# Optimization experiments

Hardware: AMD Instinct MI355X
Metric: run time of the kernel (lower is better)

## Reference

```python
import jax, jax.numpy as jnp
import numpy as np

N_NODES = 50000
N_EDGES = 800000
N_GRAPHS = 512
NNF = 32      # num_node_features
EAD = 16      # edge_attr_dim
UD = 32       # u_dim
H = 64        # hidden_dim
OUT = 1


def _w(key, shape, scale=0.05):
    return (jax.random.normal(key, shape, dtype=jnp.float32) * scale)


def setup_inputs() -> dict:
    key = jax.random.key(0)
    ks = iter(jax.random.split(key, 64))
    inp = {
        "x": jax.random.normal(next(ks), (N_NODES, NNF), dtype=jnp.float32),
        "edge_attr": jax.random.normal(next(ks), (N_EDGES, EAD), dtype=jnp.float32),
        "u": jax.random.normal(next(ks), (N_GRAPHS, UD), dtype=jnp.float32),
        # edge MLPs: Linear(EAD,H), ReLU, Linear(H,H)
        "em1_w1": _w(next(ks), (EAD, H)), "em1_b1": jnp.zeros((H,), jnp.float32),
        "em1_w2": _w(next(ks), (H, H)),   "em1_b2": jnp.zeros((H,), jnp.float32),
        "em2_w1": _w(next(ks), (EAD, H)), "em2_b1": jnp.zeros((H,), jnp.float32),
        "em2_w2": _w(next(ks), (H, H)),   "em2_b2": jnp.zeros((H,), jnp.float32),
        # layer-1 GINEConvs (a,b,c stacked on leading axis 3):
        # internal edge projection lin: Linear(H -> NNF); nn: Linear(NNF,H),ReLU,Linear(H,H)
        "c1_lin_w": _w(next(ks), (3, H, NNF)), "c1_lin_b": jnp.zeros((3, NNF), jnp.float32),
        "c1_w1": _w(next(ks), (3, NNF, H)),    "c1_b1": jnp.zeros((3, H), jnp.float32),
        "c1_w2": _w(next(ks), (3, H, H)),      "c1_b2": jnp.zeros((3, H), jnp.float32),
        # layer-2 GINEConvs: lin: Linear(H->H); nn: Linear(H,H),ReLU,Linear(H,H)
        "c2_lin_w": _w(next(ks), (3, H, H)), "c2_lin_b": jnp.zeros((3, H), jnp.float32),
        "c2_w1": _w(next(ks), (3, H, H)),    "c2_b1": jnp.zeros((3, H), jnp.float32),
        "c2_w2": _w(next(ks), (3, H, H)),    "c2_b2": jnp.zeros((3, H), jnp.float32),
        # fusion linears and head
        "lin1_w": _w(next(ks), (3 * H, H)), "lin1_b": jnp.zeros((H,), jnp.float32),
        "lin2_w": _w(next(ks), (3 * H, H)), "lin2_b": jnp.zeros((H,), jnp.float32),
        "fc_w": _w(next(ks), (H + UD, OUT)), "fc_b": jnp.zeros((OUT,), jnp.float32),
        "edge_index": jax.random.randint(next(ks), (2, N_EDGES), 0, N_NODES, dtype=jnp.int64),
        "batch": jnp.sort(jax.random.randint(next(ks), (N_NODES,), 0, N_GRAPHS, dtype=jnp.int64)),
    }
    return inp


def _gine(x, src, dst, ea, lin_w, lin_b, w1, b1, w2, b2):
    # GINEConv (eps=0): out = nn(x + sum_j relu(x_j + lin(e_ij)))
    m = jax.nn.relu(x[src] + ea @ lin_w + lin_b)          # [E, d_x]
    agg = jax.ops.segment_sum(m, dst, num_segments=x.shape[0])
    h = x + agg
    return jax.nn.relu(h @ w1 + b1) @ w2 + b2             # [N, H]


def _triple(x, src, dst, ea, lw, lb, w1, b1, w2, b2):
    # run 3 parallel GINEConvs (a,b,c) and concat features
    outs = jax.vmap(_gine, in_axes=(None, None, None, None, 0, 0, 0, 0, 0, 0))(
        x, src, dst, ea, lw, lb, w1, b1, w2, b2)          # [3, N, H]
    return outs.transpose(1, 0, 2).reshape(x.shape[0], -1)  # [N, 3H]


def reference(x, edge_attr, u,
              em1_w1, em1_b1, em1_w2, em1_b2,
              em2_w1, em2_b1, em2_w2, em2_b2,
              c1_lin_w, c1_lin_b, c1_w1, c1_b1, c1_w2, c1_b2,
              c2_lin_w, c2_lin_b, c2_w1, c2_b1, c2_w2, c2_b2,
              lin1_w, lin1_b, lin2_w, lin2_b, fc_w, fc_b,
              edge_index, batch):
    src, dst = edge_index[0], edge_index[1]
    # layer 1
    ea1 = jax.nn.relu(edge_attr @ em1_w1 + em1_b1) @ em1_w2 + em1_b2
    h = _triple(x, src, dst, ea1, c1_lin_w, c1_lin_b, c1_w1, c1_b1, c1_w2, c1_b2)
    h = jax.nn.relu(h @ lin1_w + lin1_b)                  # [N, H]
    # layer 2
    ea2 = jax.nn.relu(edge_attr @ em2_w1 + em2_b1) @ em2_w2 + em2_b2
    h = _triple(h, src, dst, ea2, c2_lin_w, c2_lin_b, c2_w1, c2_b1, c2_w2, c2_b2)
    h = jax.nn.relu(h @ lin2_w + lin2_b)                  # [N, H]
    # global mean pool per graph
    sums = jax.ops.segment_sum(h, batch, num_segments=N_GRAPHS)
    cnt = jax.ops.segment_sum(jnp.ones((h.shape[0], 1), h.dtype), batch, num_segments=N_GRAPHS)
    pooled = sums / jnp.maximum(cnt, 1.0)                 # [G, H]
    return jnp.concatenate([pooled, u], axis=-1) @ fc_w + fc_b  # [G, 1]
```

## Files before the change

### kernel.cpp

```cpp
#include <hip/hip_runtime.h>
#include <hip/hip_bf16.h>

#define N_NODES  50000
#define N_EDGES  800000
#define N_GRAPHS 512
#define ECHUNK   400000
#define NTILES   3125

typedef short bf16x8 __attribute__((ext_vector_type(8)));
typedef float f32x4  __attribute__((ext_vector_type(4)));
typedef float f32x2  __attribute__((ext_vector_type(2)));

constexpr size_t B_CNT  = 0;
constexpr size_t ZERO_BYTES = 200192;
constexpr size_t B_OFF  = 200192;
constexpr size_t B_CUR  = 400384;
constexpr size_t B_BSUM = 600576;
constexpr size_t B_SSRC = 601600;
constexpr size_t B_SEID = 3801600;
constexpr size_t B_FR2  = 7001600;
constexpr size_t B_AGG2 = 7134720;
constexpr size_t B_Q    = 45534720;
constexpr size_t B_H1   = 199134720;
constexpr size_t B_H2   = 211934720;
constexpr size_t B_FOLD = 224734720;
constexpr size_t B_FRAG = 224908416;
constexpr int F_V1H = 0;
constexpr int F_B1F = 6144;
constexpr int F_V2H = 6240;
constexpr int F_B2F = 18528;
constexpr int F_U1  = 18720;
constexpr int F_UB1 = 31008;
constexpr int F_U2  = 31072;
constexpr int F_UB2 = 43360;
constexpr int FOLD_TOTAL = 43424;
constexpr int FR_W1E1 = 0;
constexpr int FR_W1E2 = 2048;
constexpr int FR_V1   = 4096;
constexpr int FR_V2   = 10240;
constexpr int FOLD2_TOTAL = 22528;
constexpr int FR3_M1W = 0;
constexpr int FR3_M1U = 6144;
constexpr int FR3_M2W = 18432;
constexpr int FR3_M2U = 30720;
constexpr int FOLD3_TOTAL = 43008;

__device__ inline unsigned short bf16u(float x) {
    unsigned int ua = __float_as_uint(x);
    return (unsigned short)((ua + 0x7FFFu + ((ua >> 16) & 1u)) >> 16);
}
__device__ inline unsigned int packbf2(float a, float b) {
    unsigned int ua = __float_as_uint(a), ub = __float_as_uint(b);
    return ((ua + 0x7FFFu + ((ua >> 16) & 1u)) >> 16) |
           ((ub + 0x7FFFu + ((ub >> 16) & 1u)) & 0xFFFF0000u);
}
__device__ inline unsigned short pkfp8(float a, float b) {
    return (unsigned short)__builtin_amdgcn_cvt_pk_fp8_f32(a, b, 0, false);
}
__device__ inline f32x2 unpkfp8(unsigned short us) {
    return __builtin_amdgcn_cvt_pk_f32_fp8((int)us, false);
}

__global__ __launch_bounds__(256) void fold_kernel(
    const float* __restrict__ em1_w2, const float* __restrict__ em1_b2,
    const float* __restrict__ em2_w2, const float* __restrict__ em2_b2,
    const float* __restrict__ c1_lin_w, const float* __restrict__ c1_lin_b,
    const float* __restrict__ c2_lin_w, const float* __restrict__ c2_lin_b,
    const float* __restrict__ c1_w2, const float* __restrict__ c1_b2,
    const float* __restrict__ c2_w2, const float* __restrict__ c2_b2,
    const float* __restrict__ lin1_w, const float* __restrict__ lin1_b,
    const float* __restrict__ lin2_w, const float* __restrict__ lin2_b,
    float* __restrict__ fw)
{
    int idx = blockIdx.x * 256 + threadIdx.x;
    if (idx >= FOLD_TOTAL) return;
    int r = idx;
    if (r < 6144) {
        int k = r / 96, c = r % 96, i = c / 32, j = c % 32;
        float s = 0.f;
        for (int m = 0; m < 64; m++) s = fmaf(em1_w2[k * 64 + m], c1_lin_w[i * 2048 + m * 32 + j], s);
        fw[F_V1H + r] = s; return;
    }
    r -= 6144;
    if (r < 96) {
        int i = r / 32, j = r % 32;
        float s = c1_lin_b[r];
        for (int m = 0; m < 64; m++) s = fmaf(em1_b2[m], c1_lin_w[i * 2048 + m * 32 + j], s);
        fw[F_B1F + r] = s; return;
    }
    r -= 96;
    if (r < 12288) {
        int k = r / 192, c = r % 192, i = c / 64, j = c % 64;
        float s = 0.f;
        for (int m = 0; m < 64; m++) s = fmaf(em2_w2[k * 64 + m], c2_lin_w[i * 4096 + m * 64 + j], s);
        fw[F_V2H + r] = s; return;
    }
    r -= 12288;
    if (r < 192) {
        int i = r / 64, j = r % 64;
        float s = c2_lin_b[r];
        for (int m = 0; m < 64; m++) s = fmaf(em2_b2[m], c2_lin_w[i * 4096 + m * 64 + j], s);
        fw[F_B2F + r] = s; return;
    }
    r -= 192;
    if (r < 12288) {
        int i = r / 4096, k = (r / 64) % 64, j = r % 64;
        float s = 0.f;
        for (int m = 0; m < 64; m++) s = fmaf(c1_w2[i * 4096 + k * 64 + m], lin1_w[(i * 64 + m) * 64 + j], s);
        fw[F_U1 + r] = s; return;
    }
    r -= 12288;
    if (r < 64) {
        float s = lin1_b[r];
        for (int i = 0; i < 3; i++)
            for (int m = 0; m < 64; m++) s = fmaf(c1_b2[i * 64 + m], lin1_w[(i * 64 + m) * 64 + r], s);
        fw[F_UB1 + r] = s; return;
    }
    r -= 64;
    if (r < 12288) {
        int i = r / 4096, k = (r / 64) % 64, j = r % 64;
        float s = 0.f;
        for (int m = 0; m < 64; m++) s = fmaf(c2_w2[i * 4096 + k * 64 + m], lin2_w[(i * 64 + m) * 64 + j], s);
        fw[F_U2 + r] = s; return;
    }
    r -= 12288;
    {
        float s = lin2_b[r];
        for (int i = 0; i < 3; i++)
            for (int m = 0; m < 64; m++) s = fmaf(c2_b2[i * 64 + m], lin2_w[(i * 64 + m) * 64 + r], s);
        fw[F_UB2 + r] = s; return;
    }
}

__global__ __launch_bounds__(256) void fold2_kernel(
    const float* __restrict__ em1_w1, const float* __restrict__ em2_w1,
    const float* __restrict__ fw, unsigned short* __restrict__ fr)
{
    int idx = blockIdx.x * 256 + threadIdx.x;
    if (idx >= FOLD2_TOTAL) return;
    if (idx < 4096) {
        const float* w = (idx < 2048) ? em1_w1 : em2_w1;
        int r = idx & 2047;
        int tt = r >> 9, lane = (r >> 3) & 63, j = r & 7;
        int q = lane >> 4, k = q * 8 + j, m = tt * 16 + (lane & 15);
        fr[idx] = (k < 16) ? bf16u(w[k * 64 + m]) : (unsigned short)0;
        return;
    }
    if (idx < 10240) {
        int r = idx - 4096;
        int nt = r / 1024, ka = (r >> 9) & 1, lane = (r >> 3) & 63, j = r & 7;
        int q = lane >> 4;
        int t = 32 * ka + 16 * (j >> 2) + 4 * q + (j & 3);
        int n = nt * 16 + (lane & 15);
        fr[idx] = bf16u(fw[F_V1H + t * 96 + n]);
        return;
    }
    {
        int r = idx - 10240;
        int nt = r / 1024, ka = (r >> 9) & 1, lane = (r >> 3) & 63, j = r & 7;
        int q = lane >> 4;
        int t = 32 * ka + 16 * (j >> 2) + 4 * q + (j & 3);
        int n = nt * 16 + (lane & 15);
        fr[idx] = bf16u(fw[F_V2H + t * 192 + n]);
        return;
    }
}

__global__ __launch_bounds__(256) void fold3_kernel(
    const float* __restrict__ c1_w1, const float* __restrict__ c2_w1,
    const float* __restrict__ fw, unsigned short* __restrict__ fr2)
{
    int idx = blockIdx.x * 256 + threadIdx.x;
    if (idx >= FOLD3_TOTAL) return;
    if (idx < 6144) {
        int i = idx / 2048, r = idx % 2048;
        int tt = r >> 9, lane = (r >> 3) & 63, jj = r & 7;
        int k = (lane >> 4) * 8 + jj, m = tt * 16 + (lane & 15);
        fr2[FR3_M1W + idx] = bf16u(c1_w1[i * 2048 + k * 64 + m]);
        return;
    }
    if (idx < 18432) {
        int r = idx - 6144;
        int i = r / 4096, r2 = r % 4096;
        int b = r2 >> 10, ka = (r2 >> 9) & 1, lane = (r2 >> 3) & 63, jj = r2 & 7;
        int t = 32 * ka + 16 * (jj >> 2) + 4 * (lane >> 4) + (jj & 3);
        int n = b * 16 + (lane & 15);
        fr2[FR3_M1U + r] = bf16u(fw[F_U1 + i * 4096 + t * 64 + n]);
        return;
    }
    if (idx < 30720) {
        int r = idx - 18432;
        int i = r / 4096, r2 = r % 4096;
        int tt = r2 >> 10, ka = (r2 >> 9) & 1, lane = (r2 >> 3) & 63, jj = r2 & 7;
        int k = ka * 32 + (lane >> 4) * 8 + jj, m = tt * 16 + (lane & 15);
        fr2[FR3_M2W + r] = bf16u(c2_w1[i * 4096 + k * 64 + m]);
        return;
    }
    {
        int r = idx - 30720;
        int i = r / 4096, r2 = r % 4096;
        int b = r2 >> 10, ka = (r2 >> 9) & 1, lane = (r2 >> 3) & 63, jj = r2 & 7;
        int t = 32 * ka + 16 * (jj >> 2) + 4 * (lane >> 4) + (jj & 3);
        int n = b * 16 + (lane & 15);
        fr2[FR3_M2U + r] = bf16u(fw[F_U2 + i * 4096 + t * 64 + n]);
        return;
    }
}

__global__ __launch_bounds__(256) void hist_kernel(const int* __restrict__ ei, int* __restrict__ cnt) {
    int e = blockIdx.x * 256 + threadIdx.x;
    if (e < N_EDGES) atomicAdd(&cnt[ei[N_EDGES + e]], 1);
}

__global__ __launch_bounds__(256) void scan1_kernel(const int* __restrict__ cnt,
                                                    int* __restrict__ off, int* __restrict__ bsum) {
    __shared__ int sh[256];
    int t = threadIdx.x, i = blockIdx.x * 256 + t;
    int v = (i < N_NODES) ? cnt[i] : 0;
    sh[t] = v; __syncthreads();
    for (int d = 1; d < 256; d <<= 1) {
        int add = (t >= d) ? sh[t - d] : 0;
        __syncthreads();
        sh[t] += add;
        __syncthreads();
    }
    if (i < N_NODES) off[i] = sh[t] - v;
    if (t == 255) bsum[blockIdx.x] = sh[255];
}

__global__ __launch_bounds__(256) void scan2_kernel(int* __restrict__ bsum) {
    __shared__ int sh[256];
    int t = threadIdx.x;
    int v = (t < 196) ? bsum[t] : 0;
    sh[t] = v; __syncthreads();
    for (int d = 1; d < 256; d <<= 1) {
        int add = (t >= d) ? sh[t - d] : 0;
        __syncthreads();
        sh[t] += add;
        __syncthreads();
    }
    bsum[t] = sh[t] - v;
}

__global__ __launch_bounds__(256) void scan3_kernel(int* __restrict__ off, const int* __restrict__ bsum,
                                                    int* __restrict__ cur) {
    int i = blockIdx.x * 256 + threadIdx.x;
    if (i < N_NODES) {
        int o = off[i] + bsum[i >> 8];
        off[i] = o;
        cur[i] = o;
    }
    if (i == 0) off[N_NODES] = N_EDGES;
}

__global__ __launch_bounds__(256) void scatter_kernel(const int* __restrict__ ei, int* __restrict__ cur,
                                                      int* __restrict__ ssrc, int* __restrict__ seid) {
    int e = blockIdx.x * 256 + threadIdx.x;
    if (e >= N_EDGES) return;
    int d = ei[N_EDGES + e];
    int p = atomicAdd(&cur[d], 1);
    ssrc[p] = ei[e];
    seid[p] = e;
}

template<int NT>
__global__ __launch_bounds__(256, 2) void edge_mfma_kernel(
    const float* __restrict__ edge_attr, const int* __restrict__ seid,
    const unsigned short* __restrict__ w1frag, const float* __restrict__ b1,
    const unsigned short* __restrict__ vfrag,  const float* __restrict__ bias2,
    unsigned short* __restrict__ qout, int tile0, int nTiles)
{
    const int lane = threadIdx.x & 63;
    const int wid  = threadIdx.x >> 6;
    const int col  = lane & 15;
    const int quad = lane >> 4;

    bf16x8 w1f[4];
#pragma unroll
    for (int tt = 0; tt < 4; tt++)
        w1f[tt] = *(const bf16x8*)(w1frag + (tt * 64 + lane) * 8);
    bf16x8 vf[NT][2];
#pragma unroll
    for (int nt = 0; nt < NT; nt++)
#pragma unroll
        for (int ka = 0; ka < 2; ka++)
            vf[nt][ka] = *(const bf16x8*)(vfrag + ((nt * 2 + ka) * 64 + lane) * 8);
    float4 b1v[4];
#pragma unroll
    for (int tt = 0; tt < 4; tt++)
        b1v[tt] = *(const float4*)(b1 + tt * 16 + quad * 4);
    float b2v[NT];
#pragma unroll
    for (int nt = 0; nt < NT; nt++) b2v[nt] = bias2[nt * 16 + col];

    const int gw = blockIdx.x * 4 + wid;
    const int stride = gridDim.x * 4;
    for (int t = gw; t < nTiles; t += stride) {
        const int s = (tile0 + t) * 16 + col;
        const int e = seid[s];
        bf16x8 eaf;
        uint4 eau = make_uint4(0u, 0u, 0u, 0u);
        if (quad < 2) {
            const float4 v0 = *(const float4*)(edge_attr + (size_t)e * 16 + quad * 8);
            const float4 v1 = *(const float4*)(edge_attr + (size_t)e * 16 + quad * 8 + 4);
            eau.x = packbf2(v0.x, v0.y); eau.y = packbf2(v0.z, v0.w);
            eau.z = packbf2(v1.x, v1.y); eau.w = packbf2(v1.z, v1.w);
        }
        eaf = __builtin_bit_cast(bf16x8, eau);

        f32x4 c1[4];
#pragma unroll
        for (int tt = 0; tt < 4; tt++) {
            f32x4 ci = {b1v[tt].x, b1v[tt].y, b1v[tt].z, b1v[tt].w};
            c1[tt] = __builtin_amdgcn_mfma_f32_16x16x32_bf16(w1f[tt], eaf, ci, 0, 0, 0);
        }

        bf16x8 a2[2];
#pragma unroll
        for (int ka = 0; ka < 2; ka++) {
            uint4 au;
            au.x = packbf2(fmaxf(c1[2 * ka][0], 0.f),     fmaxf(c1[2 * ka][1], 0.f));
            au.y = packbf2(fmaxf(c1[2 * ka][2], 0.f),     fmaxf(c1[2 * ka][3], 0.f));
            au.z = packbf2(fmaxf(c1[2 * ka + 1][0], 0.f), fmaxf(c1[2 * ka + 1][1], 0.f));
            au.w = packbf2(fmaxf(c1[2 * ka + 1][2], 0.f), fmaxf(c1[2 * ka + 1][3], 0.f));
            a2[ka] = __builtin_bit_cast(bf16x8, au);
        }

        f32x4 c2[NT];
#pragma unroll
        for (int nt = 0; nt < NT; nt++) {
            f32x4 ci = {b2v[nt], b2v[nt], b2v[nt], b2v[nt]};
            ci = __builtin_amdgcn_mfma_f32_16x16x32_bf16(a2[0], vf[nt][0], ci, 0, 0, 0);
            c2[nt] = __builtin_amdgcn_mfma_f32_16x16x32_bf16(a2[1], vf[nt][1], ci, 0, 0, 0);
        }

        const size_t rowb = (size_t)t * 16 + quad * 4;
#pragma unroll
        for (int b = 0; b < NT / 2; b++) {
#pragma unroll
            for (int r = 0; r < 4; r++) {
                qout[(rowb + r) * (size_t)(NT * 8) + b * 16 + col] =
                    pkfp8(c2[2 * b][r], c2[2 * b + 1][r]);
            }
        }
    }
}

__global__ __launch_bounds__(64) void gather1_kernel(
    const float* __restrict__ x, const int* __restrict__ off, const int* __restrict__ ssrc,
    const unsigned short* __restrict__ q1, float* __restrict__ agg1)
{
    const int n = blockIdx.x, l = threadIdx.x;
    if (l >= 48) return;
    const int s0 = off[n], s1 = off[n + 1];
    const int c = l & 15;
    const int n1 = (l >> 4) * 32 + c, n2 = n1 + 16;
    float a0 = 0.f, a1 = 0.f, b0 = 0.f, b1 = 0.f;
    int s = s0;
    for (; s + 2 <= s1; s += 2) {
        const int srcA = ssrc[s], srcB = ssrc[s + 1];
        const unsigned short uA = q1[(size_t)s * 48 + l];
        const unsigned short uB = q1[(size_t)(s + 1) * 48 + l];
        const float xA0 = x[(size_t)srcA * 32 + c], xA1 = x[(size_t)srcA * 32 + c + 16];
        const float xB0 = x[(size_t)srcB * 32 + c], xB1 = x[(size_t)srcB * 32 + c + 16];
        const f32x2 dA = unpkfp8(uA);
        const f32x2 dB = unpkfp8(uB);
        a0 += fmaxf(xA0 + dA.x, 0.f);
        a1 += fmaxf(xA1 + dA.y, 0.f);
        b0 += fmaxf(xB0 + dB.x, 0.f);
        b1 += fmaxf(xB1 + dB.y, 0.f);
    }
    if (s < s1) {
        const int src = ssrc[s];
        const f32x2 d = unpkfp8(q1[(size_t)s * 48 + l]);
        a0 += fmaxf(x[(size_t)src * 32 + c] + d.x, 0.f);
        a1 += fmaxf(x[(size_t)src * 32 + c + 16] + d.y, 0.f);
    }
    agg1[(size_t)n * 96 + n1] = a0 + b0;
    agg1[(size_t)n * 96 + n2] = a1 + b1;
}

__global__ __launch_bounds__(256) void mlp1_mfma_kernel(
    const float* __restrict__ x, const float* __restrict__ agg1,
    const unsigned short* __restrict__ fr2, const float* __restrict__ c1_b1,
    const float* __restrict__ fw, float* __restrict__ h1)
{
    const int lane = threadIdx.x & 63, wid = threadIdx.x >> 6;
    const int tile = blockIdx.x * 4 + wid;
    if (tile >= NTILES) return;
    const int col = lane & 15, quad = lane >> 4;
    const int node = tile * 16 + col;

    const float4 xa = *(const float4*)(x + (size_t)node * 32 + quad * 8);
    const float4 xb = *(const float4*)(x + (size_t)node * 32 + quad * 8 + 4);

    f32x4 c2[4];
#pragma unroll
    for (int b = 0; b < 4; b++) {
        const float ub = fw[F_UB1 + b * 16 + col];
        c2[b] = {ub, ub, ub, ub};
    }
#pragma unroll
    for (int i = 0; i < 3; i++) {
        const float4 a0 = *(const float4*)(agg1 + (size_t)node * 96 + i * 32 + quad * 8);
        const float4 a1 = *(const float4*)(agg1 + (size_t)node * 96 + i * 32 + quad * 8 + 4);
        uint4 iu;
        iu.x = packbf2(xa.x + a0.x, xa.y + a0.y);
        iu.y = packbf2(xa.z + a0.z, xa.w + a0.w);
        iu.z = packbf2(xb.x + a1.x, xb.y + a1.y);
        iu.w = packbf2(xb.z + a1.z, xb.w + a1.w);
        const bf16x8 inf = __builtin_bit_cast(bf16x8, iu);

        f32x4 c1[4];
#pragma unroll
        for (int tt = 0; tt < 4; tt++) {
            const bf16x8 wf = *(const bf16x8*)(fr2 + FR3_M1W + ((i * 4 + tt) * 64 + lane) * 8);
            const float4 bi = *(const float4*)(c1_b1 + i * 64 + tt * 16 + quad * 4);
            f32x4 ci = {bi.x, bi.y, bi.z, bi.w};
            c1[tt] = __builtin_amdgcn_mfma_f32_16x16x32_bf16(wf, inf, ci, 0, 0, 0);
        }
        bf16x8 a2[2];
#pragma unroll
        for (int ka = 0; ka < 2; ka++) {
            uint4 au;
            au.x = packbf2(fmaxf(c1[2 * ka][0], 0.f),     fmaxf(c1[2 * ka][1], 0.f));
            au.y = packbf2(fmaxf(c1[2 * ka][2], 0.f),     fmaxf(c1[2 * ka][3], 0.f));
            au.z = packbf2(fmaxf(c1[2 * ka + 1][0], 0.f), fmaxf(c1[2 * ka + 1][1], 0.f));
            au.w = packbf2(fmaxf(c1[2 * ka + 1][2], 0.f), fmaxf(c1[2 * ka + 1][3], 0.f));
            a2[ka] = __builtin_bit_cast(bf16x8, au);
        }
#pragma unroll
        for (int b = 0; b < 4; b++)
#pragma unroll
            for (int ka = 0; ka < 2; ka++) {
                const bf16x8 uf = *(const bf16x8*)(fr2 + FR3_M1U + (((i * 4 + b) * 2 + ka) * 64 + lane) * 8);
                c2[b] = __builtin_amdgcn_mfma_f32_16x16x32_bf16(a2[ka], uf, c2[b], 0, 0, 0);
            }
    }
    const int rowb = tile * 16 + quad * 4;
#pragma unroll
    for (int b = 0; b < 4; b++)
#pragma unroll
        for (int r = 0; r < 4; r++)
            h1[(size_t)(rowb + r) * 64 + b * 16 + col] = fmaxf(c2[b][r], 0.f);
}

__global__ __launch_bounds__(64) void gather2_kernel(
    const float* __restrict__ h1, const int* __restrict__ off, const int* __restrict__ ssrc,
    const unsigned short* __restrict__ q2, float* __restrict__ agg2, int lo, int hi, int first)
{
    const int n = blockIdx.x, l = threadIdx.x;
    int s0 = off[n], s1 = off[n + 1];
    if (s0 < lo) s0 = lo;
    if (s1 > hi) s1 = hi;
    if (!first && s0 >= s1) return;

    const int k1 = ((l >> 4) & 1) * 32 + (l & 15);
    float sa0 = 0.f, sa1 = 0.f, sb0 = 0.f, sb1 = 0.f;
    float ta0 = 0.f, ta1 = 0.f, tb0 = 0.f, tb1 = 0.f;
    int s = s0;
    for (; s + 2 <= s1; s += 2) {
        const int srcA = ssrc[s], srcB = ssrc[s + 1];
        const float hA0 = h1[(size_t)srcA * 64 + k1];
        const float hA1 = h1[(size_t)srcA * 64 + k1 + 16];
        const float hB0 = h1[(size_t)srcB * 64 + k1];
        const float hB1 = h1[(size_t)srcB * 64 + k1 + 16];
        const f32x2 dA = unpkfp8(q2[(size_t)(s - lo) * 96 + l]);
        const f32x2 dB = unpkfp8(q2[(size_t)(s + 1 - lo) * 96 + l]);
        sa0 += fmaxf(hA0 + dA.x, 0.f);
        sa1 += fmaxf(hA1 + dA.y, 0.f);
        ta0 += fmaxf(hB0 + dB.x, 0.f);
        ta1 += fmaxf(hB1 + dB.y, 0.f);
        if (l < 32) {
            const f32x2 d2A = unpkfp8(q2[(size_t)(s - lo) * 96 + 64 + l]);
            const f32x2 d2B = unpkfp8(q2[(size_t)(s + 1 - lo) * 96 + 64 + l]);
            sb0 += fmaxf(hA0 + d2A.x, 0.f);
            sb1 += fmaxf(hA1 + d2A.y, 0.f);
            tb0 += fmaxf(hB0 + d2B.x, 0.f);
            tb1 += fmaxf(hB1 + d2B.y, 0.f);
        }
    }
    if (s < s1) {
        const int src = ssrc[s];
        const float hv0 = h1[(size_t)src * 64 + k1];
        const float hv1 = h1[(size_t)src * 64 + k1 + 16];
        const f32x2 d = unpkfp8(q2[(size_t)(s - lo) * 96 + l]);
        sa0 += fmaxf(hv0 + d.x, 0.f);
        sa1 += fmaxf(hv1 + d.y, 0.f);
        if (l < 32) {
            const f32x2 d2 = unpkfp8(q2[(size_t)(s - lo) * 96 + 64 + l]);
            sb0 += fmaxf(hv0 + d2.x, 0.f);
            sb1 += fmaxf(hv1 + d2.y, 0.f);
        }
    }
    sa0 += ta0; sa1 += ta1; sb0 += tb0; sb1 += tb1;
    const int C1 = 32 * (l >> 4) + (l & 15);
    const int C2 = 128 + 32 * (l >> 4) + (l & 15);
    float* row = agg2 + (size_t)n * 192;
    if (first) {
        row[C1] = sa0; row[C1 + 16] = sa1;
        if (l < 32) { row[C2] = sb0; row[C2 + 16] = sb1; }
    } else {
        row[C1] += sa0; row[C1 + 16] += sa1;
        if (l < 32) { row[C2] += sb0; row[C2 + 16] += sb1; }
    }
}

__global__ __launch_bounds__(256) void mlp2_mfma_kernel(
    const float* __restrict__ h1, const float* __restrict__ agg2,
    const unsigned short* __restrict__ fr2, const float* __restrict__ c2_b1,
    const float* __restrict__ fw, float* __restrict__ h2)
{
    const int lane = threadIdx.x & 63, wid = threadIdx.x >> 6;
    const int tile = blockIdx.x * 4 + wid;
    if (tile >= NTILES) return;
    const int col = lane & 15, quad = lane >> 4;
    const int node = tile * 16 + col;

    float4 hv[4];
#pragma unroll
    for (int p = 0; p < 4; p++)
        hv[p] = *(const float4*)(h1 + (size_t)node * 64 + (p >> 1) * 32 + quad * 8 + (p & 1) * 4);

    f32x4 c2[4];
#pragma unroll
    for (int b = 0; b < 4; b++) {
        const float ub = fw[F_UB2 + b * 16 + col];
        c2[b] = {ub, ub, ub, ub};
    }
#pragma unroll
    for (int i = 0; i < 3; i++) {
        bf16x8 inf[2];
#pragma unroll
        for (int ka = 0; ka < 2; ka++) {
            const float4 a0 = *(const float4*)(agg2 + (size_t)node * 192 + i * 64 + ka * 32 + quad * 8);
            const float4 a1 = *(const float4*)(agg2 + (size_t)node * 192 + i * 64 + ka * 32 + quad * 8 + 4);
            const float4 h0 = hv[ka * 2], h1v = hv[ka * 2 + 1];
            uint4 iu;
            iu.x = packbf2(h0.x + a0.x, h0.y + a0.y);
            iu.y = packbf2(h0.z + a0.z, h0.w + a0.w);
            iu.z = packbf2(h1v.x + a1.x, h1v.y + a1.y);
            iu.w = packbf2(h1v.z + a1.z, h1v.w + a1.w);
            inf[ka] = __builtin_bit_cast(bf16x8, iu);
        }
        f32x4 c1[4];
#pragma unroll
        for (int tt = 0; tt < 4; tt++) {
            const bf16x8 wf0 = *(const bf16x8*)(fr2 + FR3_M2W + (((i * 4 + tt) * 2 + 0) * 64 + lane) * 8);
            const bf16x8 wf1 = *(const bf16x8*)(fr2 + FR3_M2W + (((i * 4 + tt) * 2 + 1) * 64 + lane) * 8);
            const float4 bi = *(const float4*)(c2_b1 + i * 64 + tt * 16 + quad * 4);
            f32x4 ci = {bi.x, bi.y, bi.z, bi.w};
            ci = __builtin_amdgcn_mfma_f32_16x16x32_bf16(wf0, inf[0], ci, 0, 0, 0);
            c1[tt] = __builtin_amdgcn_mfma_f32_16x16x32_bf16(wf1, inf[1], ci, 0, 0, 0);
        }
        bf16x8 a2[2];
#pragma unroll
        for (int ka = 0; ka < 2; ka++) {
            uint4 au;
            au.x = packbf2(fmaxf(c1[2 * ka][0], 0.f),     fmaxf(c1[2 * ka][1], 0.f));
            au.y = packbf2(fmaxf(c1[2 * ka][2], 0.f),     fmaxf(c1[2 * ka][3], 0.f));
            au.z = packbf2(fmaxf(c1[2 * ka + 1][0], 0.f), fmaxf(c1[2 * ka + 1][1], 0.f));
            au.w = packbf2(fmaxf(c1[2 * ka + 1][2], 0.f), fmaxf(c1[2 * ka + 1][3], 0.f));
            a2[ka] = __builtin_bit_cast(bf16x8, au);
        }
#pragma unroll
        for (int b = 0; b < 4; b++)
#pragma unroll
            for (int ka = 0; ka < 2; ka++) {
                const bf16x8 uf = *(const bf16x8*)(fr2 + FR3_M2U + (((i * 4 + b) * 2 + ka) * 64 + lane) * 8);
                c2[b] = __builtin_amdgcn_mfma_f32_16x16x32_bf16(a2[ka], uf, c2[b], 0, 0, 0);
            }
    }
    const int rowb = tile * 16 + quad * 4;
#pragma unroll
    for (int b = 0; b < 4; b++)
#pragma unroll
        for (int r = 0; r < 4; r++)
            h2[(size_t)(rowb + r) * 64 + b * 16 + col] = fmaxf(c2[b][r], 0.f);
}

__global__ __launch_bounds__(256) void pool_kernel(
    const float* __restrict__ h2, const int* __restrict__ batch,
    const float* __restrict__ u, const float* __restrict__ fc_w,
    const float* __restrict__ fc_b, float* __restrict__ out)
{
    __shared__ float red[256];
    const int g = blockIdx.x, t = threadIdx.x;
    int lo = 0, hi = N_NODES;
    while (lo < hi) { int m = (lo + hi) >> 1; if (batch[m] < g) lo = m + 1; else hi = m; }
    int lo2 = lo, hi2 = N_NODES;
    while (lo2 < hi2) { int m = (lo2 + hi2) >> 1; if (batch[m] < g + 1) lo2 = m + 1; else hi2 = m; }

    const int col = t & 63, ch = t >> 6;
    float s = 0.f;
    for (int idx = lo + ch; idx < lo2; idx += 4) s += h2[(size_t)idx * 64 + col];
    red[t] = s;
    __syncthreads();
    if (t < 64) red[t] = red[t] + red[64 + t] + red[128 + t] + red[192 + t];
    __syncthreads();
    if (t == 0) {
        const float inv = 1.f / fmaxf((float)(lo2 - lo), 1.f);
        float sv = fc_b[0];
        for (int j = 0; j < 64; j++) sv = fmaf(red[j] * inv, fc_w[j], sv);
        for (int k = 0; k < 32; k++) sv = fmaf(u[(size_t)g * 32 + k], fc_w[64 + k], sv);
        out[g] = sv;
    }
}

extern "C" void kernel_launch(void* const* d_in, const int* in_sizes, int n_in,
                              void* d_out, int out_size, void* d_ws, size_t ws_size,
                              hipStream_t stream) {
    (void)in_sizes; (void)n_in; (void)out_size; (void)ws_size;
    const float* x        = (const float*)d_in[0];
    const float* edge_attr= (const float*)d_in[1];
    const float* u        = (const float*)d_in[2];
    const float* em1_w1   = (const float*)d_in[3];
    const float* em1_b1   = (const float*)d_in[4];
    const float* em1_w2   = (const float*)d_in[5];
    const float* em1_b2   = (const float*)d_in[6];
    const float* em2_w1   = (const float*)d_in[7];
    const float* em2_b1   = (const float*)d_in[8];
    const float* em2_w2   = (const float*)d_in[9];
    const float* em2_b2   = (const float*)d_in[10];
    const float* c1_lin_w = (const float*)d_in[11];
    const float* c1_lin_b = (const float*)d_in[12];
    const float* c1_w1    = (const float*)d_in[13];
    const float* c1_b1    = (const float*)d_in[14];
    const float* c1_w2    = (const float*)d_in[15];
    const float* c1_b2    = (const float*)d_in[16];
    const float* c2_lin_w = (const float*)d_in[17];
    const float* c2_lin_b = (const float*)d_in[18];
    const float* c2_w1    = (const float*)d_in[19];
    const float* c2_b1    = (const float*)d_in[20];
    const float* c2_w2    = (const float*)d_in[21];
    const float* c2_b2    = (const float*)d_in[22];
    const float* lin1_w   = (const float*)d_in[23];
    const float* lin1_b   = (const float*)d_in[24];
    const float* lin2_w   = (const float*)d_in[25];
    const float* lin2_b   = (const float*)d_in[26];
    const float* fc_w     = (const float*)d_in[27];
    const float* fc_b     = (const float*)d_in[28];
    const int*   ei       = (const int*)d_in[29];
    const int*   batch    = (const int*)d_in[30];

    char* wsb = (char*)d_ws;
    int*   cnt  = (int*)(wsb + B_CNT);
    int*   off  = (int*)(wsb + B_OFF);
    int*   cur  = (int*)(wsb + B_CUR);
    int*   bsum = (int*)(wsb + B_BSUM);
    int*   ssrc = (int*)(wsb + B_SSRC);
    int*   seid = (int*)(wsb + B_SEID);
    float* agg2 = (float*)(wsb + B_AGG2);
    unsigned short* q = (unsigned short*)(wsb + B_Q);
    float* h1   = (float*)(wsb + B_H1);
    float* h2   = (float*)(wsb + B_H2);
    float* fw   = (float*)(wsb + B_FOLD);
    unsigned short* fr  = (unsigned short*)(wsb + B_FRAG);
    unsigned short* fr2 = (unsigned short*)(wsb + B_FR2);
    float* out  = (float*)d_out;

    (void)hipMemsetAsync(d_ws, 0, ZERO_BYTES, stream);

    fold_kernel<<<(FOLD_TOTAL + 255) / 256, 256, 0, stream>>>(
        em1_w2, em1_b2, em2_w2, em2_b2, c1_lin_w, c1_lin_b, c2_lin_w, c2_lin_b,
        c1_w2, c1_b2, c2_w2, c2_b2, lin1_w, lin1_b, lin2_w, lin2_b, fw);
    fold2_kernel<<<(FOLD2_TOTAL + 255) / 256, 256, 0, stream>>>(em1_w1, em2_w1, fw, fr);
    fold3_kernel<<<(FOLD3_TOTAL + 255) / 256, 256, 0, stream>>>(c1_w1, c2_w1, fw, fr2);

    hist_kernel<<<N_EDGES / 256, 256, 0, stream>>>(ei, cnt);
    scan1_kernel<<<196, 256, 0, stream>>>(cnt, off, bsum);
    scan2_kernel<<<1, 256, 0, stream>>>(bsum);
    scan3_kernel<<<196, 256, 0, stream>>>(off, bsum, cur);
    scatter_kernel<<<N_EDGES / 256, 256, 0, stream>>>(ei, cur, ssrc, seid);

    edge_mfma_kernel<6><<<2048, 256, 0, stream>>>(
        edge_attr, seid, fr + FR_W1E1, em1_b1, fr + FR_V1, fw + F_B1F, q, 0, N_EDGES / 16);
    gather1_kernel<<<N_NODES, 64, 0, stream>>>(x, off, ssrc, q, agg2);
    mlp1_mfma_kernel<<<(NTILES + 3) / 4, 256, 0, stream>>>(x, agg2, fr2, c1_b1, fw, h1);

    for (int c = 0; c < 2; c++) {
        const int lo = c * ECHUNK, hi = lo + ECHUNK;
        edge_mfma_kernel<12><<<1024, 256, 0, stream>>>(
            edge_attr, seid, fr + FR_W1E2, em2_b1, fr + FR_V2, fw + F_B2F, q,
            lo / 16, ECHUNK / 16);
        gather2_kernel<<<N_NODES, 64, 0, stream>>>(h1, off, ssrc, q, agg2, lo, hi, c == 0 ? 1 : 0);
    }
    mlp2_mfma_kernel<<<(NTILES + 3) / 4, 256, 0, stream>>>(h1, agg2, fr2, c2_b1, fw, h2);

    pool_kernel<<<N_GRAPHS, 256, 0, stream>>>(h2, batch, u, fc_w, fc_b, out);
}
```

Measured before the change: 503.4 us.

## Process layer-2 edges in one pass and interleave sorted src/edge-id arrays

Drops the two-chunk split of the layer-2 edge MLP and gather. The layer-2 edge MLP now runs once over all 800k edges into the full q buffer, then a single gather2 writes agg2 directly. This removes a second gather2 launch over every node and the read-modify-write accumulation into agg2. It also merges the separate ssrc and seid arrays into one int2 array written by scatter. The gathers now load 8 bytes per edge where they only need the source index, and the full-size intermediate buffer raises peak workspace use.

```diff
diff --git a/kernel.cpp b/kernel.cpp
--- a/kernel.cpp
+++ b/kernel.cpp
@@ -4,7 +4,6 @@
 #define N_NODES  50000
 #define N_EDGES  800000
 #define N_GRAPHS 512
-#define ECHUNK   400000
 #define NTILES   3125
 
 typedef short bf16x8 __attribute__((ext_vector_type(8)));
@@ -16,8 +15,7 @@
 constexpr size_t B_OFF  = 200192;
 constexpr size_t B_CUR  = 400384;
 constexpr size_t B_BSUM = 600576;
-constexpr size_t B_SSRC = 601600;
-constexpr size_t B_SEID = 3801600;
+constexpr size_t B_SEDGE= 601600;
 constexpr size_t B_FR2  = 7001600;
 constexpr size_t B_AGG2 = 7134720;
 constexpr size_t B_Q    = 45534720;
@@ -254,21 +252,20 @@
 }
 
 __global__ __launch_bounds__(256) void scatter_kernel(const int* __restrict__ ei, int* __restrict__ cur,
-                                                      int* __restrict__ ssrc, int* __restrict__ seid) {
+                                                      int2* __restrict__ sedge) {
     int e = blockIdx.x * 256 + threadIdx.x;
     if (e >= N_EDGES) return;
     int d = ei[N_EDGES + e];
     int p = atomicAdd(&cur[d], 1);
-    ssrc[p] = ei[e];
-    seid[p] = e;
+    sedge[p] = make_int2(ei[e], e);
 }
 
 template<int NT>
 __global__ __launch_bounds__(256, 2) void edge_mfma_kernel(
-    const float* __restrict__ edge_attr, const int* __restrict__ seid,
+    const float* __restrict__ edge_attr, const int2* __restrict__ sedge,
     const unsigned short* __restrict__ w1frag, const float* __restrict__ b1,
     const unsigned short* __restrict__ vfrag,  const float* __restrict__ bias2,
-    unsigned short* __restrict__ qout, int tile0, int nTiles)
+    unsigned short* __restrict__ qout, int nTiles)
 {
     const int lane = threadIdx.x & 63;
     const int wid  = threadIdx.x >> 6;
@@ -296,8 +293,8 @@
     const int gw = blockIdx.x * 4 + wid;
     const int stride = gridDim.x * 4;
     for (int t = gw; t < nTiles; t += stride) {
-        const int s = (tile0 + t) * 16 + col;
-        const int e = seid[s];
+        const int s = t * 16 + col;
+        const int e = sedge[s].y;
         bf16x8 eaf;
         uint4 eau = make_uint4(0u, 0u, 0u, 0u);
         if (quad < 2) {
@@ -347,7 +344,7 @@
 }
 
 __global__ __launch_bounds__(64) void gather1_kernel(
-    const float* __restrict__ x, const int* __restrict__ off, const int* __restrict__ ssrc,
+    const float* __restrict__ x, const int* __restrict__ off, const int2* __restrict__ sedge,
     const unsigned short* __restrict__ q1, float* __restrict__ agg1)
 {
     const int n = blockIdx.x, l = threadIdx.x;
@@ -358,7 +355,7 @@
     float a0 = 0.f, a1 = 0.f, b0 = 0.f, b1 = 0.f;
     int s = s0;
     for (; s + 2 <= s1; s += 2) {
-        const int srcA = ssrc[s], srcB = ssrc[s + 1];
+        const int srcA = sedge[s].x, srcB = sedge[s + 1].x;
         const unsigned short uA = q1[(size_t)s * 48 + l];
         const unsigned short uB = q1[(size_t)(s + 1) * 48 + l];
         const float xA0 = x[(size_t)srcA * 32 + c], xA1 = x[(size_t)srcA * 32 + c + 16];
@@ -371,7 +368,7 @@
         b1 += fmaxf(xB1 + dB.y, 0.f);
     }
     if (s < s1) {
-        const int src = ssrc[s];
+        const int src = sedge[s].x;
         const f32x2 d = unpkfp8(q1[(size_t)s * 48 + l]);
         a0 += fmaxf(x[(size_t)src * 32 + c] + d.x, 0.f);
         a1 += fmaxf(x[(size_t)src * 32 + c + 16] + d.y, 0.f);
@@ -446,34 +443,31 @@
 }
 
 __global__ __launch_bounds__(64) void gather2_kernel(
-    const float* __restrict__ h1, const int* __restrict__ off, const int* __restrict__ ssrc,
-    const unsigned short* __restrict__ q2, float* __restrict__ agg2, int lo, int hi, int first)
+    const float* __restrict__ h1, const int* __restrict__ off, const int2* __restrict__ sedge,
+    const unsigned short* __restrict__ q2, float* __restrict__ agg2)
 {
     const int n = blockIdx.x, l = threadIdx.x;
-    int s0 = off[n], s1 = off[n + 1];
-    if (s0 < lo) s0 = lo;
-    if (s1 > hi) s1 = hi;
-    if (!first && s0 >= s1) return;
+    const int s0 = off[n], s1 = off[n + 1];
 
     const int k1 = ((l >> 4) & 1) * 32 + (l & 15);
     float sa0 = 0.f, sa1 = 0.f, sb0 = 0.f, sb1 = 0.f;
     float ta0 = 0.f, ta1 = 0.f, tb0 = 0.f, tb1 = 0.f;
     int s = s0;
     for (; s + 2 <= s1; s += 2) {
-        const int srcA = ssrc[s], srcB = ssrc[s + 1];
+        const int srcA = sedge[s].x, srcB = sedge[s + 1].x;
         const float hA0 = h1[(size_t)srcA * 64 + k1];
         const float hA1 = h1[(size_t)srcA * 64 + k1 + 16];
         const float hB0 = h1[(size_t)srcB * 64 + k1];
         const float hB1 = h1[(size_t)srcB * 64 + k1 + 16];
-        const f32x2 dA = unpkfp8(q2[(size_t)(s - lo) * 96 + l]);
-        const f32x2 dB = unpkfp8(q2[(size_t)(s + 1 - lo) * 96 + l]);
+        const f32x2 dA = unpkfp8(q2[(size_t)s * 96 + l]);
+        const f32x2 dB = unpkfp8(q2[(size_t)(s + 1) * 96 + l]);
         sa0 += fmaxf(hA0 + dA.x, 0.f);
         sa1 += fmaxf(hA1 + dA.y, 0.f);
         ta0 += fmaxf(hB0 + dB.x, 0.f);
         ta1 += fmaxf(hB1 + dB.y, 0.f);
         if (l < 32) {
-            const f32x2 d2A = unpkfp8(q2[(size_t)(s - lo) * 96 + 64 + l]);
-            const f32x2 d2B = unpkfp8(q2[(size_t)(s + 1 - lo) * 96 + 64 + l]);
+            const f32x2 d2A = unpkfp8(q2[(size_t)s * 96 + 64 + l]);
+            const f32x2 d2B = unpkfp8(q2[(size_t)(s + 1) * 96 + 64 + l]);
             sb0 += fmaxf(hA0 + d2A.x, 0.f);
             sb1 += fmaxf(hA1 + d2A.y, 0.f);
             tb0 += fmaxf(hB0 + d2B.x, 0.f);
@@ -481,14 +475,14 @@
         }
     }
     if (s < s1) {
-        const int src = ssrc[s];
+        const int src = sedge[s].x;
         const float hv0 = h1[(size_t)src * 64 + k1];
         const float hv1 = h1[(size_t)src * 64 + k1 + 16];
-        const f32x2 d = unpkfp8(q2[(size_t)(s - lo) * 96 + l]);
+        const f32x2 d = unpkfp8(q2[(size_t)s * 96 + l]);
         sa0 += fmaxf(hv0 + d.x, 0.f);
         sa1 += fmaxf(hv1 + d.y, 0.f);
         if (l < 32) {
-            const f32x2 d2 = unpkfp8(q2[(size_t)(s - lo) * 96 + 64 + l]);
+            const f32x2 d2 = unpkfp8(q2[(size_t)s * 96 + 64 + l]);
             sb0 += fmaxf(hv0 + d2.x, 0.f);
             sb1 += fmaxf(hv1 + d2.y, 0.f);
         }
@@ -497,13 +491,8 @@
     const int C1 = 32 * (l >> 4) + (l & 15);
     const int C2 = 128 + 32 * (l >> 4) + (l & 15);
     float* row = agg2 + (size_t)n * 192;
-    if (first) {
-        row[C1] = sa0; row[C1 + 16] = sa1;
-        if (l < 32) { row[C2] = sb0; row[C2 + 16] = sb1; }
-    } else {
-        row[C1] += sa0; row[C1 + 16] += sa1;
-        if (l < 32) { row[C2] += sb0; row[C2 + 16] += sb1; }
-    }
+    row[C1] = sa0; row[C1 + 16] = sa1;
+    if (l < 32) { row[C2] = sb0; row[C2 + 16] = sb1; }
 }
 
 __global__ __launch_bounds__(256) void mlp2_mfma_kernel(
@@ -648,8 +637,7 @@
     int*   off  = (int*)(wsb + B_OFF);
     int*   cur  = (int*)(wsb + B_CUR);
     int*   bsum = (int*)(wsb + B_BSUM);
-    int*   ssrc = (int*)(wsb + B_SSRC);
-    int*   seid = (int*)(wsb + B_SEID);
+    int2*  sedge= (int2*)(wsb + B_SEDGE);
     float* agg2 = (float*)(wsb + B_AGG2);
     unsigned short* q = (unsigned short*)(wsb + B_Q);
     float* h1   = (float*)(wsb + B_H1);
@@ -671,20 +659,16 @@
     scan1_kernel<<<196, 256, 0, stream>>>(cnt, off, bsum);
     scan2_kernel<<<1, 256, 0, stream>>>(bsum);
     scan3_kernel<<<196, 256, 0, stream>>>(off, bsum, cur);
-    scatter_kernel<<<N_EDGES / 256, 256, 0, stream>>>(ei, cur, ssrc, seid);
+    scatter_kernel<<<N_EDGES / 256, 256, 0, stream>>>(ei, cur, sedge);
 
     edge_mfma_kernel<6><<<2048, 256, 0, stream>>>(
-        edge_attr, seid, fr + FR_W1E1, em1_b1, fr + FR_V1, fw + F_B1F, q, 0, N_EDGES / 16);
-    gather1_kernel<<<N_NODES, 64, 0, stream>>>(x, off, ssrc, q, agg2);
+        edge_attr, sedge, fr + FR_W1E1, em1_b1, fr + FR_V1, fw + F_B1F, q, N_EDGES / 16);
+    gather1_kernel<<<N_NODES, 64, 0, stream>>>(x, off, sedge, q, agg2);
     mlp1_mfma_kernel<<<(NTILES + 3) / 4, 256, 0, stream>>>(x, agg2, fr2, c1_b1, fw, h1);
 
-    for (int c = 0; c < 2; c++) {
-        const int lo = c * ECHUNK, hi = lo + ECHUNK;
-        edge_mfma_kernel<12><<<1024, 256, 0, stream>>>(
-            edge_attr, seid, fr + FR_W1E2, em2_b1, fr + FR_V2, fw + F_B2F, q,
-            lo / 16, ECHUNK / 16);
-        gather2_kernel<<<N_NODES, 64, 0, stream>>>(h1, off, ssrc, q, agg2, lo, hi, c == 0 ? 1 : 0);
-    }
+    edge_mfma_kernel<12><<<2048, 256, 0, stream>>>(
+        edge_attr, sedge, fr + FR_W1E2, em2_b1, fr + FR_V2, fw + F_B2F, q, N_EDGES / 16);
+    gather2_kernel<<<N_NODES, 64, 0, stream>>>(h1, off, sedge, q, agg2);
     mlp2_mfma_kernel<<<(NTILES + 3) / 4, 256, 0, stream>>>(h1, agg2, fr2, c2_b1, fw, h2);
 
     pool_kernel<<<N_GRAPHS, 256, 0, stream>>>(h2, batch, u, fc_w, fc_b, out);
```

New measurement: 488.7 us. 2.9% less time.
